# Kernel optimization log

Hardware: AMD Instinct MI355X
Metric: run time of the kernel (lower is better)

The kernel has to match this reference:

```python
import jax, jax.numpy as jnp
import numpy as np

N = 100000  # num nodes
E = 1600000  # num edges
D_IN = 128
D_HID = 128
D_OUT = 128


def setup_inputs() -> dict:
    key = jax.random.key(0)
    ks = jax.random.split(key, 8)
    x1 = jax.random.normal(ks[0], (N, D_IN), dtype=jnp.float32)
    x2 = jax.random.normal(ks[1], (N, D_IN), dtype=jnp.float32)
    ei1 = jax.random.randint(ks[2], (2, E), 0, N, dtype=jnp.int64)
    ei2 = jax.random.randint(ks[3], (2, E), 0, N, dtype=jnp.int64)
    s0 = 1.0 / np.sqrt(D_IN)
    s1 = 1.0 / np.sqrt(D_HID)
    W0 = jax.random.normal(ks[4], (D_IN, D_HID), dtype=jnp.float32) * s0
    b0 = jnp.zeros((D_HID,), dtype=jnp.float32)
    W1 = jax.random.normal(ks[5], (D_HID, D_OUT), dtype=jnp.float32) * s1
    b1 = jnp.zeros((D_OUT,), dtype=jnp.float32)
    return {"x1": x1, "edge_index1": ei1, "x2": x2, "edge_index2": ei2,
            "W0": W0, "b0": b0, "W1": W1, "b1": b1}


def _gcn_conv(x, edge_index, W, b):
    # PyG GCNConv: add self-loops, symmetric normalization deg^{-1/2}(A+I)deg^{-1/2}
    src, dst = edge_index[0], edge_index[1]
    h = x @ W  # [N, d_out] -- transform before propagate (PyG default)
    # degree on A + I (self-loop contributes 1)
    deg = jax.ops.segment_sum(jnp.ones_like(src, dtype=h.dtype), dst, num_segments=N) + 1.0
    dinv = jax.lax.rsqrt(deg)  # [N]
    norm = dinv[src] * dinv[dst]  # [E]
    agg = jax.ops.segment_sum(h[src] * norm[:, None], dst, num_segments=N)
    agg = agg + h * (dinv * dinv)[:, None]  # self-loop message
    return agg + b


def reference(x1, edge_index1, x2, edge_index2, W0, b0, W1, b1):
    def backbone(x, ei):
        h = jax.nn.relu(_gcn_conv(x, ei, W0, b0))
        return _gcn_conv(h, ei, W1, b1)

    h1 = backbone(x1, edge_index1)
    h2 = backbone(x2, edge_index2)
    return (h1, h2)
```

## Files before the change

kernel.cpp:

```cpp
#include <hip/hip_runtime.h>
#include <hip/hip_bf16.h>

#define NN 100000
#define NE 1600000
#define DIM 128
#define NBLK ((NN + 255) / 256)

#define NSLICE 8
#define SLICE_N 12500
#define NCHUNK 128
#define CHUNK_E 12500

using bf16 = __hip_bfloat16;
using bf162 = __hip_bfloat162;

__device__ __forceinline__ float to_f(const float v) { return v; }
__device__ __forceinline__ float to_f(const bf16 v) { return __bfloat162float(v); }

__device__ __forceinline__ float4 ld4(const float* p) {
    return *reinterpret_cast<const float4*>(p);
}
__device__ __forceinline__ float4 ld4(const bf16* p) {
    const bf162* q = reinterpret_cast<const bf162*>(p);
    float2 a = __bfloat1622float2(q[0]);
    float2 b = __bfloat1622float2(q[1]);
    return make_float4(a.x, a.y, b.x, b.y);
}
__device__ __forceinline__ void ld8(const float* p, float4& a, float4& b) {
    a = *reinterpret_cast<const float4*>(p);
    b = *reinterpret_cast<const float4*>(p + 4);
}
__device__ __forceinline__ void ld8(const bf16* p, float4& a, float4& b) {
    float4 r = *reinterpret_cast<const float4*>(p);
    const bf162* q = reinterpret_cast<const bf162*>(&r);
    float2 f0 = __bfloat1622float2(q[0]);
    float2 f1 = __bfloat1622float2(q[1]);
    float2 f2 = __bfloat1622float2(q[2]);
    float2 f3 = __bfloat1622float2(q[3]);
    a = make_float4(f0.x, f0.y, f1.x, f1.y);
    b = make_float4(f2.x, f2.y, f3.x, f3.y);
}
__device__ __forceinline__ void st1(float* p, float v) { *p = v; }
__device__ __forceinline__ void st1(bf16* p, float v) { *p = __float2bfloat16(v); }
__device__ __forceinline__ void st4(float* p, float4 v) {
    *reinterpret_cast<float4*>(p) = v;
}
__device__ __forceinline__ void st4(bf16* p, float4 v) {
    bf162* q = reinterpret_cast<bf162*>(p);
    q[0] = __float22bfloat162_rn(make_float2(v.x, v.y));
    q[1] = __float22bfloat162_rn(make_float2(v.z, v.w));
}

__global__ __launch_bounds__(256) void count_deg_k(const int* __restrict__ dst,
                                                   int* __restrict__ cnt) {
    const int s = blockIdx.x & 7;
    const int c = blockIdx.x >> 3;
    const int lo = s * SLICE_N;
    const int beg = c * CHUNK_E, end = beg + CHUNK_E;
    for (int e = beg + threadIdx.x; e < end; e += 256) {
        int d = dst[e];
        if ((unsigned)(d - lo) < (unsigned)SLICE_N) atomicAdd(&cnt[d], 1);
    }
}

__global__ void dinv_k(const int* __restrict__ cnt, float* __restrict__ dinv) {
    int i = blockIdx.x * blockDim.x + threadIdx.x;
    if (i < NN) dinv[i] = rsqrtf((float)cnt[i] + 1.0f);
}

__global__ void blocksum_k(const int* __restrict__ cnt, int* __restrict__ bsum) {
    __shared__ int s[256];
    int i = blockIdx.x * 256 + threadIdx.x;
    s[threadIdx.x] = (i < NN) ? cnt[i] : 0;
    __syncthreads();
    for (int off = 128; off > 0; off >>= 1) {
        if (threadIdx.x < off) s[threadIdx.x] += s[threadIdx.x + off];
        __syncthreads();
    }
    if (threadIdx.x == 0) bsum[blockIdx.x] = s[0];
}

__global__ void scan_bsum_k(const int* __restrict__ bsum, int* __restrict__ boff) {
    __shared__ int s[512];
    int t = threadIdx.x;
    int v = (t < NBLK) ? bsum[t] : 0;
    s[t] = v;
    __syncthreads();
    for (int off = 1; off < 512; off <<= 1) {
        int tmp = (t >= off) ? s[t - off] : 0;
        __syncthreads();
        s[t] += tmp;
        __syncthreads();
    }
    if (t < NBLK) boff[t] = s[t] - v;
}

__global__ void scan_block_k(const int* __restrict__ cnt, const int* __restrict__ boff,
                             int* __restrict__ row_ptr, int* __restrict__ cursor) {
    __shared__ int s[256];
    int t = threadIdx.x, i = blockIdx.x * 256 + t;
    int v = (i < NN) ? cnt[i] : 0;
    s[t] = v;
    __syncthreads();
    for (int off = 1; off < 256; off <<= 1) {
        int tmp = (t >= off) ? s[t - off] : 0;
        __syncthreads();
        s[t] += tmp;
        __syncthreads();
    }
    if (i < NN) {
        int e = boff[blockIdx.x] + s[t] - v;
        row_ptr[i] = e;
        cursor[i] = e;
    }
    if (i == NN - 1) row_ptr[NN] = NE;
}

__global__ __launch_bounds__(256) void fill_k(const int* __restrict__ src,
                                              const int* __restrict__ dst,
                                              int* __restrict__ cursor,
                                              int* __restrict__ csr_src) {
    const int s = blockIdx.x & 7;
    const int c = blockIdx.x >> 3;
    const int lo = s * SLICE_N;
    const int beg = c * CHUNK_E, end = beg + CHUNK_E;
    for (int e = beg + threadIdx.x; e < end; e += 256) {
        int d = dst[e];
        if ((unsigned)(d - lo) < (unsigned)SLICE_N) {
            int pos = atomicAdd(&cursor[d], 1);
            csr_src[pos] = src[e];
        }
    }
}

template <typename ST, typename OT, bool RELU>
__global__ __launch_bounds__(256) void fused_gg_k(const int* __restrict__ row_ptr,
                                                  const int* __restrict__ csr_src,
                                                  const float* __restrict__ dinv,
                                                  const ST* __restrict__ h,
                                                  const float* __restrict__ W,
                                                  const float* __restrict__ bias,
                                                  OT* __restrict__ out) {
    __shared__ float xs[32][DIM];
    const int t = threadIdx.x;
    const int r0 = blockIdx.x * 32;
    const int wv = t >> 6;
    const int lane = t & 63;
    const int q = lane >> 4;
    const int m = lane & 15;

    for (int i = 0; i < 8; ++i) {
        const int nd = r0 + wv * 8 + i;
        const int beg = row_ptr[nd], end = row_ptr[nd + 1];
        const float dd = dinv[nd];
        float4 A0 = make_float4(0.f, 0.f, 0.f, 0.f);
        float4 A1 = A0;
        for (int base = beg; base < end; base += 64) {
            int k = end - base;
            if (k > 64) k = 64;
            int s = 0;
            float ns = 0.f;
            if (lane < k) { s = csr_src[base + lane]; ns = dinv[s]; }
            const int kfull = k & ~7;
            for (int j = 0; j < kfull; j += 8) {
                int   s0 = __shfl(s,  j + q);
                float n0 = __shfl(ns, j + q);
                int   s1 = __shfl(s,  j + 4 + q);
                float n1 = __shfl(ns, j + 4 + q);
                float4 a0, b0, a1, b1;
                ld8(&h[(size_t)s0 * DIM + m * 8], a0, b0);
                ld8(&h[(size_t)s1 * DIM + m * 8], a1, b1);
                A0.x = fmaf(a0.x, n0, A0.x);
                A0.y = fmaf(a0.y, n0, A0.y);
                A0.z = fmaf(a0.z, n0, A0.z);
                A0.w = fmaf(a0.w, n0, A0.w);
                A1.x = fmaf(b0.x, n0, A1.x);
                A1.y = fmaf(b0.y, n0, A1.y);
                A1.z = fmaf(b0.z, n0, A1.z);
                A1.w = fmaf(b0.w, n0, A1.w);
                A0.x = fmaf(a1.x, n1, A0.x);
                A0.y = fmaf(a1.y, n1, A0.y);
                A0.z = fmaf(a1.z, n1, A0.z);
                A0.w = fmaf(a1.w, n1, A0.w);
                A1.x = fmaf(b1.x, n1, A1.x);
                A1.y = fmaf(b1.y, n1, A1.y);
                A1.z = fmaf(b1.z, n1, A1.z);
                A1.w = fmaf(b1.w, n1, A1.w);
            }
            if (kfull < k) {
                int   s0 = __shfl(s,  kfull + q);
                float n0 = __shfl(ns, kfull + q);
                float4 a0, b0;
                ld8(&h[(size_t)s0 * DIM + m * 8], a0, b0);
                if (kfull + 4 < k) {
                    int   s1 = __shfl(s,  kfull + 4 + q);
                    float n1 = __shfl(ns, kfull + 4 + q);
                    float4 a1, b1;
                    ld8(&h[(size_t)s1 * DIM + m * 8], a1, b1);
                    A0.x = fmaf(a1.x, n1, A0.x);
                    A0.y = fmaf(a1.y, n1, A0.y);
                    A0.z = fmaf(a1.z, n1, A0.z);
                    A0.w = fmaf(a1.w, n1, A0.w);
                    A1.x = fmaf(b1.x, n1, A1.x);
                    A1.y = fmaf(b1.y, n1, A1.y);
                    A1.z = fmaf(b1.z, n1, A1.z);
                    A1.w = fmaf(b1.w, n1, A1.w);
                }
                A0.x = fmaf(a0.x, n0, A0.x);
                A0.y = fmaf(a0.y, n0, A0.y);
                A0.z = fmaf(a0.z, n0, A0.z);
                A0.w = fmaf(a0.w, n0, A0.w);
                A1.x = fmaf(b0.x, n0, A1.x);
                A1.y = fmaf(b0.y, n0, A1.y);
                A1.z = fmaf(b0.z, n0, A1.z);
                A1.w = fmaf(b0.w, n0, A1.w);
            }
        }
        A0.x += __shfl_xor(A0.x, 16); A0.y += __shfl_xor(A0.y, 16);
        A0.z += __shfl_xor(A0.z, 16); A0.w += __shfl_xor(A0.w, 16);
        A1.x += __shfl_xor(A1.x, 16); A1.y += __shfl_xor(A1.y, 16);
        A1.z += __shfl_xor(A1.z, 16); A1.w += __shfl_xor(A1.w, 16);
        A0.x += __shfl_xor(A0.x, 32); A0.y += __shfl_xor(A0.y, 32);
        A0.z += __shfl_xor(A0.z, 32); A0.w += __shfl_xor(A0.w, 32);
        A1.x += __shfl_xor(A1.x, 32); A1.y += __shfl_xor(A1.y, 32);
        A1.z += __shfl_xor(A1.z, 32); A1.w += __shfl_xor(A1.w, 32);
        if (q == 0) {
            float4 sa, sb;
            ld8(&h[(size_t)nd * DIM + m * 8], sa, sb);
            float d2 = dd * dd;
            float4 v0 = make_float4(fmaf(sa.x, d2, A0.x * dd),
                                    fmaf(sa.y, d2, A0.y * dd),
                                    fmaf(sa.z, d2, A0.z * dd),
                                    fmaf(sa.w, d2, A0.w * dd));
            float4 v1 = make_float4(fmaf(sb.x, d2, A1.x * dd),
                                    fmaf(sb.y, d2, A1.y * dd),
                                    fmaf(sb.z, d2, A1.z * dd),
                                    fmaf(sb.w, d2, A1.w * dd));
            *reinterpret_cast<float4*>(&xs[wv * 8 + i][m * 8]) = v0;
            *reinterpret_cast<float4*>(&xs[wv * 8 + i][m * 8 + 4]) = v1;
        }
    }
    __syncthreads();

    const int cw = t & 31;
    const int rb = (t >> 5) * 4;
    const float4* __restrict__ Wv = reinterpret_cast<const float4*>(W);

    float4 acc0 = make_float4(0.f, 0.f, 0.f, 0.f);
    float4 acc1 = acc0, acc2 = acc0, acc3 = acc0;

#pragma unroll 4
    for (int k = 0; k < DIM; ++k) {
        float4 w = Wv[k * 32 + cw];
        float x0 = xs[rb + 0][k];
        float x1 = xs[rb + 1][k];
        float x2 = xs[rb + 2][k];
        float x3 = xs[rb + 3][k];
        acc0.x = fmaf(x0, w.x, acc0.x);
        acc0.y = fmaf(x0, w.y, acc0.y);
        acc0.z = fmaf(x0, w.z, acc0.z);
        acc0.w = fmaf(x0, w.w, acc0.w);
        acc1.x = fmaf(x1, w.x, acc1.x);
        acc1.y = fmaf(x1, w.y, acc1.y);
        acc1.z = fmaf(x1, w.z, acc1.z);
        acc1.w = fmaf(x1, w.w, acc1.w);
        acc2.x = fmaf(x2, w.x, acc2.x);
        acc2.y = fmaf(x2, w.y, acc2.y);
        acc2.z = fmaf(x2, w.z, acc2.z);
        acc2.w = fmaf(x2, w.w, acc2.w);
        acc3.x = fmaf(x3, w.x, acc3.x);
        acc3.y = fmaf(x3, w.y, acc3.y);
        acc3.z = fmaf(x3, w.z, acc3.z);
        acc3.w = fmaf(x3, w.w, acc3.w);
    }

    float4 b4 = *reinterpret_cast<const float4*>(&bias[cw * 4]);
    auto fin = [&](float4 a) {
        a.x += b4.x; a.y += b4.y; a.z += b4.z; a.w += b4.w;
        if (RELU) {
            a.x = fmaxf(a.x, 0.f); a.y = fmaxf(a.y, 0.f);
            a.z = fmaxf(a.z, 0.f); a.w = fmaxf(a.w, 0.f);
        }
        return a;
    };
    size_t o = (size_t)(r0 + rb) * DIM + cw * 4;
    st4(&out[o], fin(acc0));
    st4(&out[o + DIM], fin(acc1));
    st4(&out[o + 2 * DIM], fin(acc2));
    st4(&out[o + 3 * DIM], fin(acc3));
}

template <typename ST>
__global__ void scatter_k(const int* __restrict__ src, const int* __restrict__ dst,
                          const float* __restrict__ dinv, const ST* __restrict__ S,
                          float* __restrict__ agg) {
    int i = blockIdx.x * blockDim.x + threadIdx.x;
    int e = i >> 5;
    int p = (i & 31) * 4;
    int s = src[e], d = dst[e];
    float nrm = dinv[s] * dinv[d];
    float4 hv = ld4(&S[(size_t)s * DIM + p]);
    float* ap = &agg[(size_t)d * DIM + p];
    atomicAdd(ap + 0, hv.x * nrm);
    atomicAdd(ap + 1, hv.y * nrm);
    atomicAdd(ap + 2, hv.z * nrm);
    atomicAdd(ap + 3, hv.w * nrm);
}

template <typename ST, typename OT, bool RELU>
__global__ __launch_bounds__(256) void gemm_fused_k(const float* agg, const ST* S,
                                                    const float* __restrict__ dinv,
                                                    const float* __restrict__ W,
                                                    const float* __restrict__ bias,
                                                    OT* out) {
    __shared__ float xs[32][DIM];
    const int t = threadIdx.x;
    const int r0 = blockIdx.x * 32;

#pragma unroll
    for (int i = 0; i < 4; ++i) {
        int idx = t + i * 256;
        int rr = idx >> 5;
        int c4 = (idx & 31) * 4;
        int r = r0 + rr;
        float di = dinv[r];
        float d2 = di * di;
        size_t off = (size_t)r * DIM + c4;
        float4 a = *reinterpret_cast<const float4*>(&agg[off]);
        float4 s = ld4(&S[off]);
        xs[rr][c4 + 0] = fmaf(s.x, d2, a.x);
        xs[rr][c4 + 1] = fmaf(s.y, d2, a.y);
        xs[rr][c4 + 2] = fmaf(s.z, d2, a.z);
        xs[rr][c4 + 3] = fmaf(s.w, d2, a.w);
    }
    __syncthreads();

    const int cw = t & 31;
    const int rb = (t >> 5) * 4;
    const float4* __restrict__ Wv = reinterpret_cast<const float4*>(W);

    float4 acc0 = make_float4(0.f, 0.f, 0.f, 0.f);
    float4 acc1 = acc0, acc2 = acc0, acc3 = acc0;

#pragma unroll 4
    for (int k = 0; k < DIM; ++k) {
        float4 w = Wv[k * 32 + cw];
        float x0 = xs[rb + 0][k];
        float x1 = xs[rb + 1][k];
        float x2 = xs[rb + 2][k];
        float x3 = xs[rb + 3][k];
        acc0.x = fmaf(x0, w.x, acc0.x);
        acc0.y = fmaf(x0, w.y, acc0.y);
        acc0.z = fmaf(x0, w.z, acc0.z);
        acc0.w = fmaf(x0, w.w, acc0.w);
        acc1.x = fmaf(x1, w.x, acc1.x);
        acc1.y = fmaf(x1, w.y, acc1.y);
        acc1.z = fmaf(x1, w.z, acc1.z);
        acc1.w = fmaf(x1, w.w, acc1.w);
        acc2.x = fmaf(x2, w.x, acc2.x);
        acc2.y = fmaf(x2, w.y, acc2.y);
        acc2.z = fmaf(x2, w.z, acc2.z);
        acc2.w = fmaf(x2, w.w, acc2.w);
        acc3.x = fmaf(x3, w.x, acc3.x);
        acc3.y = fmaf(x3, w.y, acc3.y);
        acc3.z = fmaf(x3, w.z, acc3.z);
        acc3.w = fmaf(x3, w.w, acc3.w);
    }

    float4 b4 = *reinterpret_cast<const float4*>(&bias[cw * 4]);
    auto fin = [&](float4 a) {
        a.x += b4.x; a.y += b4.y; a.z += b4.z; a.w += b4.w;
        if (RELU) {
            a.x = fmaxf(a.x, 0.f); a.y = fmaxf(a.y, 0.f);
            a.z = fmaxf(a.z, 0.f); a.w = fmaxf(a.w, 0.f);
        }
        return a;
    };
    size_t o = (size_t)(r0 + rb) * DIM + cw * 4;
    st4(&out[o], fin(acc0));
    st4(&out[o + DIM], fin(acc1));
    st4(&out[o + 2 * DIM], fin(acc2));
    st4(&out[o + 3 * DIM], fin(acc3));
}

__global__ void compress8_k(const float* __restrict__ src, bf16* __restrict__ dst) {
    size_t i = (size_t)blockIdx.x * blockDim.x + threadIdx.x;
    const float4* s = reinterpret_cast<const float4*>(src) + i * 2;
    float4 a = s[0], b = s[1];
    bf162 r[4];
    r[0] = __float22bfloat162_rn(make_float2(a.x, a.y));
    r[1] = __float22bfloat162_rn(make_float2(a.z, a.w));
    r[2] = __float22bfloat162_rn(make_float2(b.x, b.y));
    r[3] = __float22bfloat162_rn(make_float2(b.z, b.w));
    *reinterpret_cast<float4*>(dst + i * 8) = *reinterpret_cast<float4*>(r);
}
__global__ void decomp_k(float* __restrict__ dst, const bf16* __restrict__ src, int n) {
    int i = blockIdx.x * blockDim.x + threadIdx.x;
    if (i < n) dst[i] = __bfloat162float(src[i]);
}

extern "C" void kernel_launch(void* const* d_in, const int* in_sizes, int n_in,
                              void* d_out, int out_size, void* d_ws, size_t ws_size,
                              hipStream_t stream) {
    const float* W0 = (const float*)d_in[4];
    const float* b0 = (const float*)d_in[5];
    const float* W1 = (const float*)d_in[6];
    const float* b1 = (const float*)d_in[7];

    char* ws = (char*)d_ws;
    int*   cnt  = (int*)ws;
    float* dinv = (float*)(ws + (512u << 10));
    int* row_ptr = (int*)(ws + (1u << 20));
    int* cursor  = (int*)(ws + (3u << 19));
    int* bsum    = (int*)(ws + (2u << 20));
    int* boff    = (int*)(ws + (2u << 20) + 4096);
    int* csr_src = (int*)(ws + (9u << 18));

    const bool csr_ok = ws_size >= (9u << 20);
    char* big = csr_ok ? ws + (9u << 20) : ws + (1u << 20);
    size_t big_avail = ws_size - (csr_ok ? (9u << 20) : (1u << 20));

    const size_t NB = (size_t)NN * DIM;
    float* slot0 = (float*)d_out;
    float* slot1 = slot0 + NB;

    const int SG = (NE * 32) / 256;
    const int GG = NN / 32;
    const int BG = NCHUNK * NSLICE;
    const int XG = (int)(NB / 2048);

    auto build = [&](const int* srcp, const int* dstp) {
        hipMemsetAsync(cnt, 0, NN * sizeof(int), stream);
        count_deg_k<<<BG, 256, 0, stream>>>(dstp, cnt);
        dinv_k<<<(NN + 255) / 256, 256, 0, stream>>>(cnt, dinv);
        if (!csr_ok) return;
        blocksum_k<<<NBLK, 256, 0, stream>>>(cnt, bsum);
        scan_bsum_k<<<1, 512, 0, stream>>>(bsum, boff);
        scan_block_k<<<NBLK, 256, 0, stream>>>(cnt, boff, row_ptr, cursor);
        fill_k<<<BG, 256, 0, stream>>>(srcp, dstp, cursor, csr_src);
    };

    if (csr_ok) {
        {
            const float* x  = (const float*)d_in[0];
            const int*   ei = (const int*)d_in[1];
            bf16* h1b = (bf16*)slot1;
            bf16* xb0 = (bf16*)((char*)slot1 + NB * sizeof(bf16));
            compress8_k<<<XG, 256, 0, stream>>>(x, xb0);
            build(ei, ei + NE);
            fused_gg_k<bf16, bf16, true><<<GG, 256, 0, stream>>>(
                row_ptr, csr_src, dinv, xb0, W0, b0, h1b);
            fused_gg_k<bf16, float, false><<<GG, 256, 0, stream>>>(
                row_ptr, csr_src, dinv, h1b, W1, b1, slot0);
        }
        {
            const float* x  = (const float*)d_in[2];
            const int*   ei = (const int*)d_in[3];
            build(ei, ei + NE);

            if (big_avail >= 2 * NB * sizeof(bf16)) {
                bf16* xb = (bf16*)big;
                bf16* H  = (bf16*)(big + NB * sizeof(bf16));
                compress8_k<<<XG, 256, 0, stream>>>(x, xb);
                fused_gg_k<bf16, bf16, true><<<GG, 256, 0, stream>>>(
                    row_ptr, csr_src, dinv, xb, W0, b0, H);
                fused_gg_k<bf16, float, false><<<GG, 256, 0, stream>>>(
                    row_ptr, csr_src, dinv, H, W1, b1, slot1);
            } else if (big_avail >= NB * sizeof(bf16)) {
                bf16* H = (bf16*)big;
                fused_gg_k<float, bf16, true><<<GG, 256, 0, stream>>>(
                    row_ptr, csr_src, dinv, x, W0, b0, H);
                fused_gg_k<bf16, float, false><<<GG, 256, 0, stream>>>(
                    row_ptr, csr_src, dinv, H, W1, b1, slot1);
            } else {
                bf16* g0b = (bf16*)slot1;
                bf16* h1b = (bf16*)((char*)slot1 + NB * sizeof(bf16));
                compress8_k<<<XG, 256, 0, stream>>>(slot0, g0b);
                fused_gg_k<float, bf16, true><<<GG, 256, 0, stream>>>(
                    row_ptr, csr_src, dinv, x, W0, b0, h1b);
                fused_gg_k<bf16, float, false><<<GG, 256, 0, stream>>>(
                    row_ptr, csr_src, dinv, h1b, W1, b1, slot0);
                float* stage = (float*)csr_src;
                size_t C = 1600000;
                size_t a = NB;
                while (a > 0) {
                    size_t len = (a >= C) ? C : a;
                    a -= len;
                    hipMemcpyAsync(stage, slot0 + a, len * sizeof(float),
                                   hipMemcpyDeviceToDevice, stream);
                    decomp_k<<<(int)((len + 255) / 256), 256, 0, stream>>>(
                        slot0 + a, g0b + a, (int)len);
                    hipMemcpyAsync(slot1 + a, stage, len * sizeof(float),
                                   hipMemcpyDeviceToDevice, stream);
                }
            }
        }
        return;
    }

    auto agg_f = [&](const int* srcp, const int* dstp, const float* h, float* agg) {
        hipMemsetAsync(agg, 0, NB * sizeof(float), stream);
        scatter_k<float><<<SG, 256, 0, stream>>>(srcp, dstp, dinv, h, agg);
    };
    auto agg_b = [&](const int* srcp, const int* dstp, const bf16* h, float* agg) {
        hipMemsetAsync(agg, 0, NB * sizeof(float), stream);
        scatter_k<bf16><<<SG, 256, 0, stream>>>(srcp, dstp, dinv, h, agg);
    };

    {
        const float* x  = (const float*)d_in[0];
        const int*   ei = (const int*)d_in[1];
        bf16* h1b = (bf16*)slot1;
        build(ei, ei + NE);
        agg_f(ei, ei + NE, x, slot0);
        gemm_fused_k<float, bf16, true><<<GG, 256, 0, stream>>>(slot0, x, dinv, W0, b0, h1b);
        agg_b(ei, ei + NE, h1b, slot0);
        gemm_fused_k<bf16, float, false><<<GG, 256, 0, stream>>>(slot0, h1b, dinv, W1, b1, slot0);
    }
    {
        const float* x  = (const float*)d_in[2];
        const int*   ei = (const int*)d_in[3];
        build(ei, ei + NE);

        bf16* g0b = (bf16*)slot1;
        bf16* h1b = (bf16*)((char*)slot1 + NB * sizeof(bf16));
        compress8_k<<<XG, 256, 0, stream>>>(slot0, g0b);
        agg_f(ei, ei + NE, x, slot0);
        gemm_fused_k<float, bf16, true><<<GG, 256, 0, stream>>>(slot0, x, dinv, W0, b0, h1b);
        agg_b(ei, ei + NE, h1b, slot0);
        gemm_fused_k<bf16, float, false><<<GG, 256, 0, stream>>>(slot0, h1b, dinv, W1, b1, slot0);
        float* stage = (float*)big;
        size_t C = (big_avail / sizeof(float)) & ~(size_t)255;
        if (C < 256) C = 256;
        size_t a = NB;
        while (a > 0) {
            size_t len = (a >= C) ? C : a;
            a -= len;
            hipMemcpyAsync(stage, slot0 + a, len * sizeof(float),
                           hipMemcpyDeviceToDevice, stream);
            decomp_k<<<(int)((len + 255) / 256), 256, 0, stream>>>(
                slot0 + a, g0b + a, (int)len);
            hipMemcpyAsync(slot1 + a, stage, len * sizeof(float),
                           hipMemcpyDeviceToDevice, stream);
        }
    }
}
```

Baseline: 946.5 us.

## Use bf16 MFMA for dense transform in fused gather-GEMM kernel

Replaces the scalar FP32 FMA loop for the 32x128 by 128x128 product in the fused gather/GEMM kernel with bf16 MFMA 16x16x32 instructions. Weights are pre-converted to bf16 in an MFMA-friendly swizzled layout by a new kernel. The aggregated rows are stored to LDS as bf16 with an XOR swizzle to avoid bank conflicts. The dinv computation is folded into the scan kernel, dropping one launch. This lowers the precision of the transform input and weights to bf16.

Result: faster. 792.9 us (-16.2%).

```diff
diff --git a/kernel.cpp b/kernel.cpp
--- a/kernel.cpp
+++ b/kernel.cpp
@@ -13,6 +13,8 @@
 
 using bf16 = __hip_bfloat16;
 using bf162 = __hip_bfloat162;
+typedef __attribute__((ext_vector_type(8))) short short8v;
+typedef __attribute__((ext_vector_type(4))) float f32x4;
 
 __device__ __forceinline__ float to_f(const float v) { return v; }
 __device__ __forceinline__ float to_f(const bf16 v) { return __bfloat162float(v); }
@@ -49,6 +51,14 @@
     bf162* q = reinterpret_cast<bf162*>(p);
     q[0] = __float22bfloat162_rn(make_float2(v.x, v.y));
     q[1] = __float22bfloat162_rn(make_float2(v.z, v.w));
+}
+__device__ __forceinline__ float4 pack8(float4 a, float4 b) {
+    bf162 r[4];
+    r[0] = __float22bfloat162_rn(make_float2(a.x, a.y));
+    r[1] = __float22bfloat162_rn(make_float2(a.z, a.w));
+    r[2] = __float22bfloat162_rn(make_float2(b.x, b.y));
+    r[3] = __float22bfloat162_rn(make_float2(b.z, b.w));
+    return *reinterpret_cast<float4*>(r);
 }
 
 __global__ __launch_bounds__(256) void count_deg_k(const int* __restrict__ dst,
@@ -96,7 +106,8 @@
 }
 
 __global__ void scan_block_k(const int* __restrict__ cnt, const int* __restrict__ boff,
-                             int* __restrict__ row_ptr, int* __restrict__ cursor) {
+                             int* __restrict__ row_ptr, int* __restrict__ cursor,
+                             float* __restrict__ dinv) {
     __shared__ int s[256];
     int t = threadIdx.x, i = blockIdx.x * 256 + t;
     int v = (i < NN) ? cnt[i] : 0;
@@ -112,6 +123,7 @@
         int e = boff[blockIdx.x] + s[t] - v;
         row_ptr[i] = e;
         cursor[i] = e;
+        dinv[i] = rsqrtf((float)v + 1.0f);
     }
     if (i == NN - 1) row_ptr[NN] = NE;
 }
@@ -133,15 +145,27 @@
     }
 }
 
+__global__ void wcvt_k(const float* __restrict__ W0, const float* __restrict__ W1,
+                       bf16* __restrict__ Wb0, bf16* __restrict__ Wb1) {
+    int idx = blockIdx.x * 256 + threadIdx.x;
+    const float* W = (idx & 16384) ? W1 : W0;
+    bf16* Wb = (idx & 16384) ? Wb1 : Wb0;
+    int e = idx & 16383;
+    int j = e & 7, l = (e >> 3) & 63, ks = (e >> 9) & 3, ct = e >> 11;
+    int k = ks * 32 + (l >> 4) * 8 + j;
+    int c = ct * 16 + (l & 15);
+    Wb[e] = __float2bfloat16(W[k * 128 + c]);
+}
+
 template <typename ST, typename OT, bool RELU>
 __global__ __launch_bounds__(256) void fused_gg_k(const int* __restrict__ row_ptr,
                                                   const int* __restrict__ csr_src,
                                                   const float* __restrict__ dinv,
                                                   const ST* __restrict__ h,
-                                                  const float* __restrict__ W,
+                                                  const bf16* __restrict__ Wb,
                                                   const float* __restrict__ bias,
                                                   OT* __restrict__ out) {
-    __shared__ float xs[32][DIM];
+    __shared__ __align__(16) bf16 xs[32][DIM];
     const int t = threadIdx.x;
     const int r0 = blockIdx.x * 32;
     const int wv = t >> 6;
@@ -227,6 +251,7 @@
         if (q == 0) {
             float4 sa, sb;
             ld8(&h[(size_t)nd * DIM + m * 8], sa, sb);
+            const int row = wv * 8 + i;
             float d2 = dd * dd;
             float4 v0 = make_float4(fmaf(sa.x, d2, A0.x * dd),
                                     fmaf(sa.y, d2, A0.y * dd),
@@ -236,9 +261,91 @@
                                     fmaf(sb.y, d2, A1.y * dd),
                                     fmaf(sb.z, d2, A1.z * dd),
                                     fmaf(sb.w, d2, A1.w * dd));
-            *reinterpret_cast<float4*>(&xs[wv * 8 + i][m * 8]) = v0;
-            *reinterpret_cast<float4*>(&xs[wv * 8 + i][m * 8 + 4]) = v1;
-        }
+            *reinterpret_cast<float4*>(&xs[row][(m ^ (row & 7)) * 8]) = pack8(v0, v1);
+        }
+    }
+    __syncthreads();
+
+    const int g  = lane >> 4;
+    const int cl = lane & 15;
+    const short8v* __restrict__ Wb8 = reinterpret_cast<const short8v*>(Wb);
+    f32x4 acc00 = {0.f, 0.f, 0.f, 0.f};
+    f32x4 acc01 = acc00, acc10 = acc00, acc11 = acc00;
+    const int ct0 = wv * 2, ct1 = wv * 2 + 1;
+#pragma unroll
+    for (int ks = 0; ks < 4; ++ks) {
+        const int u = (ks * 4 + g) ^ (cl & 7);
+        short8v a0 = *reinterpret_cast<const short8v*>(&xs[cl][u * 8]);
+        short8v a1 = *reinterpret_cast<const short8v*>(&xs[16 + cl][u * 8]);
+        short8v b0 = Wb8[(ct0 * 4 + ks) * 64 + lane];
+        short8v b1 = Wb8[(ct1 * 4 + ks) * 64 + lane];
+        acc00 = __builtin_amdgcn_mfma_f32_16x16x32_bf16(a0, b0, acc00, 0, 0, 0);
+        acc01 = __builtin_amdgcn_mfma_f32_16x16x32_bf16(a0, b1, acc01, 0, 0, 0);
+        acc10 = __builtin_amdgcn_mfma_f32_16x16x32_bf16(a1, b0, acc10, 0, 0, 0);
+        acc11 = __builtin_amdgcn_mfma_f32_16x16x32_bf16(a1, b1, acc11, 0, 0, 0);
+    }
+    const int colb = wv * 32 + cl;
+    const float bb0 = bias[colb];
+    const float bb1 = bias[colb + 16];
+#pragma unroll
+    for (int r = 0; r < 4; ++r) {
+        int row_a = r0 + g * 4 + r;
+        int row_b = r0 + 16 + g * 4 + r;
+        float v00 = acc00[r] + bb0, v01 = acc01[r] + bb1;
+        float v10 = acc10[r] + bb0, v11 = acc11[r] + bb1;
+        if (RELU) {
+            v00 = fmaxf(v00, 0.f); v01 = fmaxf(v01, 0.f);
+            v10 = fmaxf(v10, 0.f); v11 = fmaxf(v11, 0.f);
+        }
+        st1(&out[(size_t)row_a * DIM + colb], v00);
+        st1(&out[(size_t)row_a * DIM + colb + 16], v01);
+        st1(&out[(size_t)row_b * DIM + colb], v10);
+        st1(&out[(size_t)row_b * DIM + colb + 16], v11);
+    }
+}
+
+template <typename ST>
+__global__ void scatter_k(const int* __restrict__ src, const int* __restrict__ dst,
+                          const float* __restrict__ dinv, const ST* __restrict__ S,
+                          float* __restrict__ agg) {
+    int i = blockIdx.x * blockDim.x + threadIdx.x;
+    int e = i >> 5;
+    int p = (i & 31) * 4;
+    int s = src[e], d = dst[e];
+    float nrm = dinv[s] * dinv[d];
+    float4 hv = ld4(&S[(size_t)s * DIM + p]);
+    float* ap = &agg[(size_t)d * DIM + p];
+    atomicAdd(ap + 0, hv.x * nrm);
+    atomicAdd(ap + 1, hv.y * nrm);
+    atomicAdd(ap + 2, hv.z * nrm);
+    atomicAdd(ap + 3, hv.w * nrm);
+}
+
+template <typename ST, typename OT, bool RELU>
+__global__ __launch_bounds__(256) void gemm_fused_k(const float* agg, const ST* S,
+                                                    const float* __restrict__ dinv,
+                                                    const float* __restrict__ W,
+                                                    const float* __restrict__ bias,
+                                                    OT* out) {
+    __shared__ float xs[32][DIM];
+    const int t = threadIdx.x;
+    const int r0 = blockIdx.x * 32;
+
+#pragma unroll
+    for (int i = 0; i < 4; ++i) {
+        int idx = t + i * 256;
+        int rr = idx >> 5;
+        int c4 = (idx & 31) * 4;
+        int r = r0 + rr;
+        float di = dinv[r];
+        float d2 = di * di;
+        size_t off = (size_t)r * DIM + c4;
+        float4 a = *reinterpret_cast<const float4*>(&agg[off]);
+        float4 s = ld4(&S[off]);
+        xs[rr][c4 + 0] = fmaf(s.x, d2, a.x);
+        xs[rr][c4 + 1] = fmaf(s.y, d2, a.y);
+        xs[rr][c4 + 2] = fmaf(s.z, d2, a.z);
+        xs[rr][c4 + 3] = fmaf(s.w, d2, a.w);
     }
     __syncthreads();
 
@@ -290,109 +397,11 @@
     st4(&out[o + 3 * DIM], fin(acc3));
 }
 
-template <typename ST>
-__global__ void scatter_k(const int* __restrict__ src, const int* __restrict__ dst,
-                          const float* __restrict__ dinv, const ST* __restrict__ S,
-                          float* __restrict__ agg) {
-    int i = blockIdx.x * blockDim.x + threadIdx.x;
-    int e = i >> 5;
-    int p = (i & 31) * 4;
-    int s = src[e], d = dst[e];
-    float nrm = dinv[s] * dinv[d];
-    float4 hv = ld4(&S[(size_t)s * DIM + p]);
-    float* ap = &agg[(size_t)d * DIM + p];
-    atomicAdd(ap + 0, hv.x * nrm);
-    atomicAdd(ap + 1, hv.y * nrm);
-    atomicAdd(ap + 2, hv.z * nrm);
-    atomicAdd(ap + 3, hv.w * nrm);
-}
-
-template <typename ST, typename OT, bool RELU>
-__global__ __launch_bounds__(256) void gemm_fused_k(const float* agg, const ST* S,
-                                                    const float* __restrict__ dinv,
-                                                    const float* __restrict__ W,
-                                                    const float* __restrict__ bias,
-                                                    OT* out) {
-    __shared__ float xs[32][DIM];
-    const int t = threadIdx.x;
-    const int r0 = blockIdx.x * 32;
-
-#pragma unroll
-    for (int i = 0; i < 4; ++i) {
-        int idx = t + i * 256;
-        int rr = idx >> 5;
-        int c4 = (idx & 31) * 4;
-        int r = r0 + rr;
-        float di = dinv[r];
-        float d2 = di * di;
-        size_t off = (size_t)r * DIM + c4;
-        float4 a = *reinterpret_cast<const float4*>(&agg[off]);
-        float4 s = ld4(&S[off]);
-        xs[rr][c4 + 0] = fmaf(s.x, d2, a.x);
-        xs[rr][c4 + 1] = fmaf(s.y, d2, a.y);
-        xs[rr][c4 + 2] = fmaf(s.z, d2, a.z);
-        xs[rr][c4 + 3] = fmaf(s.w, d2, a.w);
-    }
-    __syncthreads();
-
-    const int cw = t & 31;
-    const int rb = (t >> 5) * 4;
-    const float4* __restrict__ Wv = reinterpret_cast<const float4*>(W);
-
-    float4 acc0 = make_float4(0.f, 0.f, 0.f, 0.f);
-    float4 acc1 = acc0, acc2 = acc0, acc3 = acc0;
-
-#pragma unroll 4
-    for (int k = 0; k < DIM; ++k) {
-        float4 w = Wv[k * 32 + cw];
-        float x0 = xs[rb + 0][k];
-        float x1 = xs[rb + 1][k];
-        float x2 = xs[rb + 2][k];
-        float x3 = xs[rb + 3][k];
-        acc0.x = fmaf(x0, w.x, acc0.x);
-        acc0.y = fmaf(x0, w.y, acc0.y);
-        acc0.z = fmaf(x0, w.z, acc0.z);
-        acc0.w = fmaf(x0, w.w, acc0.w);
-        acc1.x = fmaf(x1, w.x, acc1.x);
-        acc1.y = fmaf(x1, w.y, acc1.y);
-        acc1.z = fmaf(x1, w.z, acc1.z);
-        acc1.w = fmaf(x1, w.w, acc1.w);
-        acc2.x = fmaf(x2, w.x, acc2.x);
-        acc2.y = fmaf(x2, w.y, acc2.y);
-        acc2.z = fmaf(x2, w.z, acc2.z);
-        acc2.w = fmaf(x2, w.w, acc2.w);
-        acc3.x = fmaf(x3, w.x, acc3.x);
-        acc3.y = fmaf(x3, w.y, acc3.y);
-        acc3.z = fmaf(x3, w.z, acc3.z);
-        acc3.w = fmaf(x3, w.w, acc3.w);
-    }
-
-    float4 b4 = *reinterpret_cast<const float4*>(&bias[cw * 4]);
-    auto fin = [&](float4 a) {
-        a.x += b4.x; a.y += b4.y; a.z += b4.z; a.w += b4.w;
-        if (RELU) {
-            a.x = fmaxf(a.x, 0.f); a.y = fmaxf(a.y, 0.f);
-            a.z = fmaxf(a.z, 0.f); a.w = fmaxf(a.w, 0.f);
-        }
-        return a;
-    };
-    size_t o = (size_t)(r0 + rb) * DIM + cw * 4;
-    st4(&out[o], fin(acc0));
-    st4(&out[o + DIM], fin(acc1));
-    st4(&out[o + 2 * DIM], fin(acc2));
-    st4(&out[o + 3 * DIM], fin(acc3));
-}
-
 __global__ void compress8_k(const float* __restrict__ src, bf16* __restrict__ dst) {
     size_t i = (size_t)blockIdx.x * blockDim.x + threadIdx.x;
     const float4* s = reinterpret_cast<const float4*>(src) + i * 2;
     float4 a = s[0], b = s[1];
-    bf162 r[4];
-    r[0] = __float22bfloat162_rn(make_float2(a.x, a.y));
-    r[1] = __float22bfloat162_rn(make_float2(a.z, a.w));
-    r[2] = __float22bfloat162_rn(make_float2(b.x, b.y));
-    r[3] = __float22bfloat162_rn(make_float2(b.z, b.w));
-    *reinterpret_cast<float4*>(dst + i * 8) = *reinterpret_cast<float4*>(r);
+    *reinterpret_cast<float4*>(dst + i * 8) = pack8(a, b);
 }
 __global__ void decomp_k(float* __restrict__ dst, const bf16* __restrict__ src, int n) {
     int i = blockIdx.x * blockDim.x + threadIdx.x;
@@ -414,6 +423,8 @@
     int* cursor  = (int*)(ws + (3u << 19));
     int* bsum    = (int*)(ws + (2u << 20));
     int* boff    = (int*)(ws + (2u << 20) + 4096);
+    bf16* Wb0    = (bf16*)(ws + (2u << 20) + 8192);
+    bf16* Wb1    = Wb0 + 16384;
     int* csr_src = (int*)(ws + (9u << 18));
 
     const bool csr_ok = ws_size >= (9u << 20);
@@ -432,15 +443,18 @@
     auto build = [&](const int* srcp, const int* dstp) {
         hipMemsetAsync(cnt, 0, NN * sizeof(int), stream);
         count_deg_k<<<BG, 256, 0, stream>>>(dstp, cnt);
-        dinv_k<<<(NN + 255) / 256, 256, 0, stream>>>(cnt, dinv);
-        if (!csr_ok) return;
+        if (!csr_ok) {
+            dinv_k<<<(NN + 255) / 256, 256, 0, stream>>>(cnt, dinv);
+            return;
+        }
         blocksum_k<<<NBLK, 256, 0, stream>>>(cnt, bsum);
         scan_bsum_k<<<1, 512, 0, stream>>>(bsum, boff);
-        scan_block_k<<<NBLK, 256, 0, stream>>>(cnt, boff, row_ptr, cursor);
+        scan_block_k<<<NBLK, 256, 0, stream>>>(cnt, boff, row_ptr, cursor, dinv);
         fill_k<<<BG, 256, 0, stream>>>(srcp, dstp, cursor, csr_src);
     };
 
     if (csr_ok) {
+        wcvt_k<<<128, 256, 0, stream>>>(W0, W1, Wb0, Wb1);
         {
             const float* x  = (const float*)d_in[0];
             const int*   ei = (const int*)d_in[1];
@@ -449,9 +463,9 @@
             compress8_k<<<XG, 256, 0, stream>>>(x, xb0);
             build(ei, ei + NE);
             fused_gg_k<bf16, bf16, true><<<GG, 256, 0, stream>>>(
-                row_ptr, csr_src, dinv, xb0, W0, b0, h1b);
+                row_ptr, csr_src, dinv, xb0, Wb0, b0, h1b);
             fused_gg_k<bf16, float, false><<<GG, 256, 0, stream>>>(
-                row_ptr, csr_src, dinv, h1b, W1, b1, slot0);
+                row_ptr, csr_src, dinv, h1b, Wb1, b1, slot0);
         }
         {
             const float* x  = (const float*)d_in[2];
@@ -463,23 +477,23 @@
                 bf16* H  = (bf16*)(big + NB * sizeof(bf16));
                 compress8_k<<<XG, 256, 0, stream>>>(x, xb);
                 fused_gg_k<bf16, bf16, true><<<GG, 256, 0, stream>>>(
-                    row_ptr, csr_src, dinv, xb, W0, b0, H);
+                    row_ptr, csr_src, dinv, xb, Wb0, b0, H);
                 fused_gg_k<bf16, float, false><<<GG, 256, 0, stream>>>(
-                    row_ptr, csr_src, dinv, H, W1, b1, slot1);
+                    row_ptr, csr_src, dinv, H, Wb1, b1, slot1);
             } else if (big_avail >= NB * sizeof(bf16)) {
                 bf16* H = (bf16*)big;
                 fused_gg_k<float, bf16, true><<<GG, 256, 0, stream>>>(
-                    row_ptr, csr_src, dinv, x, W0, b0, H);
+                    row_ptr, csr_src, dinv, x, Wb0, b0, H);
                 fused_gg_k<bf16, float, false><<<GG, 256, 0, stream>>>(
-                    row_ptr, csr_src, dinv, H, W1, b1, slot1);
+                    row_ptr, csr_src, dinv, H, Wb1, b1, slot1);
             } else {
                 bf16* g0b = (bf16*)slot1;
                 bf16* h1b = (bf16*)((char*)slot1 + NB * sizeof(bf16));
                 compress8_k<<<XG, 256, 0, stream>>>(slot0, g0b);
                 fused_gg_k<float, bf16, true><<<GG, 256, 0, stream>>>(
-                    row_ptr, csr_src, dinv, x, W0, b0, h1b);
+                    row_ptr, csr_src, dinv, x, Wb0, b0, h1b);
                 fused_gg_k<bf16, float, false><<<GG, 256, 0, stream>>>(
-                    row_ptr, csr_src, dinv, h1b, W1, b1, slot0);
+                    row_ptr, csr_src, dinv, h1b, Wb1, b1, slot0);
                 float* stage = (float*)csr_src;
                 size_t C = 1600000;
                 size_t a = NB;
```
